# Kernel optimization log

Hardware: AMD Instinct MI355X
Metric: run time of the kernel (lower is better)

Reference implementation:

```python
import jax, jax.numpy as jnp
import numpy as np

SR = 44100
B, T = 4, SR * 3          # batch, samples (duration_secs=3)
NWT, L = 64, 512          # n_wavetables, wavetable_len


def setup_inputs() -> dict:
    key = jax.random.key(0)
    k1, k2, k3, k4, k5 = jax.random.split(key, 5)
    pitch = jax.random.uniform(k1, (B, T, 1), dtype=jnp.float32, minval=50.0, maxval=500.0)
    amplitude = jax.random.uniform(k2, (B, T, 1), dtype=jnp.float32)
    y = jax.random.normal(k3, (B, T), dtype=jnp.float32)
    wavetables = jax.random.normal(k4, (NWT, L), dtype=jnp.float32) * 0.01
    # replicate init: last sample equals first sample of each table
    wavetables = wavetables.at[:, -1].set(wavetables[:, 0])
    conv_w = jax.random.normal(k5, (1, 1, 5), dtype=jnp.float32) * 0.3  # Conv1d(1,1,5)
    conv_b = jnp.zeros((1,), dtype=jnp.float32)
    return {"pitch": pitch, "amplitude": amplitude, "y": y,
            "wavetables": wavetables, "conv_w": conv_w, "conv_b": conv_b,
            "duration_secs": 3}


def reference(pitch, amplitude, y, wavetables, conv_w, conv_b, duration_secs):
    Lwt = wavetables.shape[1]
    freq = pitch.squeeze(-1)                                   # (B, T)
    increment = freq / SR * Lwt                                # (B, T)
    # NOTE: faithful to source: subtract batch-row 0 from every row
    index = jnp.cumsum(increment, axis=1) - increment[0]
    index = index % Lwt
    idx_low = jnp.floor(index)
    idx_high = jnp.ceil(index)
    alpha = index - idx_low                                    # (B, T)
    il = idx_low.astype(jnp.int32)
    ih = idx_high.astype(jnp.int32) % Lwt
    # vectorized over all 64 wavetables at once (source loops in Python)
    low = jnp.take(wavetables, il, axis=1)                     # (N, B, T)
    high = jnp.take(wavetables, ih, axis=1)                    # (N, B, T)
    waveforms = low + alpha * (high - low)                     # (N, B, T)
    # attention: mean over batch of waveform * y
    att = jnp.mean(waveforms * y, axis=1)                      # (N, T)
    att = jax.lax.conv_general_dilated(
        att[:, None, :], conv_w, window_strides=(1,), padding=[(2, 2)],
        dimension_numbers=("NCH", "OIH", "NCH"))[:, 0, :] + conv_b[0]
    att = jax.nn.softmax(att, axis=0)                          # softmax over wavetables
    out = jnp.einsum("nbt,nt->bt", waveforms, att)             # (B, T)
    out = out[..., None] * amplitude                           # (B, T, 1)
    return out
```

## Files before the change

kernel.cpp:

```cpp
#include <hip/hip_runtime.h>
#include <math.h>

#define LWT 512
#define NWT 64
#define BB 4
#define SBASE 16
#define BLK 128
#define HALO 132


#define INC_C ((float)(512.0 / 44100.0))

__device__ __forceinline__ float inc_mul(float p) {
  float v = p * INC_C;
  asm volatile("" : "+v"(v));
  return v;
}
__device__ __forceinline__ float inc_of(const float* p, int t) { return inc_mul(p[t]); }

__global__ void __launch_bounds__(256) scan_level0(const float* __restrict__ pitch,
                                                   float* __restrict__ sarr,
                                                   float* __restrict__ s1g,
                                                   const float* __restrict__ wt,
                                                   float* __restrict__ wtT,
                                                   int T, int NB1) {
  if (blockIdx.y == BB) {
    int i = blockIdx.x * blockDim.x + threadIdx.x;
    if (i < NWT * LWT) {
      int n = i >> 9, c = i & 511;
      wtT[c * NWT + n] = wt[i];
    }
    return;
  }
  int k = blockIdx.x * blockDim.x + threadIdx.x;
  int b = blockIdx.y;
  if (k >= NB1) return;
  const float* prow = pitch + (size_t)b * T;
  float* srow = sarr + (size_t)b * T;
  int t0 = k * SBASE;
  float run = 0.0f;
  if (t0 + SBASE <= T) {
    const float4* p4 = reinterpret_cast<const float4*>(prow + t0);
    float4* s4o = reinterpret_cast<float4*>(srow + t0);
#pragma unroll
    for (int i = 0; i < 4; ++i) {
      float4 v = p4[i];
      float4 o;
      run += inc_mul(v.x); o.x = run;
      run += inc_mul(v.y); o.y = run;
      run += inc_mul(v.z); o.z = run;
      run += inc_mul(v.w); o.w = run;
      s4o[i] = o;
    }
  } else {
    for (int t = t0; t < T; ++t) { run += inc_of(prow, t); srow[t] = run; }
  }
  s1g[(size_t)b * NB1 + k] = run;
}

__global__ void __launch_bounds__(1024) scan_upper(float* __restrict__ s1g, int NB1) {
  int b = blockIdx.x;
  int tid = threadIdx.x;
  float* s1r = s1g + (size_t)b * NB1;
  __shared__ float s1[8320];
  __shared__ float s2[544];
  __shared__ float s3[48];
  __shared__ float s4[16];
  const int NB2 = (NB1 + SBASE - 1) / SBASE;
  const int NB3 = (NB2 + SBASE - 1) / SBASE;
  const int NB4 = (NB3 + SBASE - 1) / SBASE;

  for (int a = tid; a < NB1; a += 1024) s1[a] = s1r[a];
  __syncthreads();
  for (int k = tid; k < NB2; k += 1024) {
    int a0 = k * SBASE, a1 = a0 + SBASE < NB1 ? a0 + SBASE : NB1;
    float run = 0.0f;
    for (int a = a0; a < a1; ++a) { run += s1[a]; s1[a] = run; }
    s2[k] = run;
  }
  __syncthreads();
  for (int k = tid; k < NB3; k += 1024) {
    int a0 = k * SBASE, a1 = a0 + SBASE < NB2 ? a0 + SBASE : NB2;
    float run = 0.0f;
    for (int a = a0; a < a1; ++a) { run += s2[a]; s2[a] = run; }
    s3[k] = run;
  }
  __syncthreads();
  for (int k = tid; k < NB4; k += 1024) {
    int a0 = k * SBASE, a1 = a0 + SBASE < NB3 ? a0 + SBASE : NB3;
    float run = 0.0f;
    for (int a = a0; a < a1; ++a) { run += s3[a]; s3[a] = run; }
    s4[k] = run;
  }
  __syncthreads();
  if (tid == 0) { float r = 0.0f; for (int a = 0; a < NB4; ++a) { r += s4[a]; s4[a] = r; } }
  __syncthreads();
  for (int a = tid; a < NB3; a += 1024)
    if (a >= SBASE) s3[a] = s3[a] + s4[a / SBASE - 1];
  __syncthreads();
  for (int a = tid; a < NB2; a += 1024)
    if (a >= SBASE) s2[a] = s2[a] + s3[a / SBASE - 1];
  __syncthreads();
  for (int a = tid; a < NB1; a += 1024) {
    float v = s1[a];
    if (a >= SBASE) v = v + s2[a / SBASE - 1];
    s1r[a] = v;
  }
}

__device__ __forceinline__ float dpp_reduce_add(float x) {
  x += __int_as_float(__builtin_amdgcn_update_dpp(0, __float_as_int(x), 0xB1, 0xf, 0xf, true));
  x += __int_as_float(__builtin_amdgcn_update_dpp(0, __float_as_int(x), 0x4E, 0xf, 0xf, true));
  x += __int_as_float(__builtin_amdgcn_update_dpp(0, __float_as_int(x), 0x141, 0xf, 0xf, true));
  x += __int_as_float(__builtin_amdgcn_update_dpp(0, __float_as_int(x), 0x140, 0xf, 0xf, true));
  x += __int_as_float(__builtin_amdgcn_update_dpp(0, __float_as_int(x), 0x142, 0xa, 0xf, true));
  x += __int_as_float(__builtin_amdgcn_update_dpp(0, __float_as_int(x), 0x143, 0xc, 0xf, true));
  return __int_as_float(__builtin_amdgcn_readlane(__float_as_int(x), 63));
}

__global__ void __launch_bounds__(512) fused_out(
    const float* __restrict__ pitch, const float* __restrict__ sarr,
    const float* __restrict__ s1g, const float* __restrict__ y,
    const float* __restrict__ amp, const float* __restrict__ wtT,
    const float* __restrict__ cw, const float* __restrict__ cb,
    float* __restrict__ out, int T, int NB1) {
  __shared__ float lds_att[HALO][64];
  __shared__ unsigned ilh_l[BB][HALO];
  __shared__ float alf_l[BB][HALO];
  __shared__ float y_l[BB][HALO];
  __shared__ float amp_l[BB][HALO];
  __shared__ float out_l[BB][BLK];
  int t0 = blockIdx.x * BLK;
  int wid = threadIdx.x >> 6, lane = threadIdx.x & 63;

  {
    int b = wid & 3;
    for (int i = (wid >> 2) * 64 + lane; i < HALO; i += 128) {
      int t = t0 - 2 + i;
      if (t >= 0 && t < T) {
        float S = sarr[(size_t)b * T + t];
        if (t >= SBASE) S = S + s1g[b * NB1 + (t >> 4) - 1];
        float iv = S - inc_of(pitch, t);
        float q = iv * (1.0f / 512.0f);
        float k = floorf(q);
        iv = fmaf(-k, 512.0f, iv);
        float fl = floorf(iv);
        float alpha = iv - fl;
        int ili = (int)fl; if (ili > 511) ili = 511;
        int ihi = ((int)ceilf(iv)) & 511;
        ilh_l[b][i] = (unsigned)ili | ((unsigned)ihi << 16);
        alf_l[b][i] = alpha;
        y_l[b][i] = y[(size_t)b * T + t];
        amp_l[b][i] = amp[(size_t)b * T + t];
      }
    }
  }
  __syncthreads();

  for (int i = wid; i < HALO; i += 8) {
    int t = t0 - 2 + i;
    float acc = 0.0f;
    if (t >= 0 && t < T) {
#pragma unroll
      for (int b = 0; b < BB; ++b) {
        unsigned st = ilh_l[b][i];
        int ili = st & 0xffff, ihi = st >> 16;
        float alpha = alf_l[b][i];
        float lo = wtT[ili * NWT + lane];
        float hi = wtT[ihi * NWT + lane];
        acc += (lo + alpha * (hi - lo)) * y_l[b][i];
      }
      acc *= 0.25f;
    }
    lds_att[i][lane] = acc;
  }
  __syncthreads();

  float w0 = cw[0], w1 = cw[1], w2 = cw[2], w3 = cw[3], w4 = cw[4];
  float bias = cb[0];
#pragma unroll 4
  for (int i = wid; i < BLK; i += 8) {
    int t = t0 + i;
    if (t >= T) continue;
    float c = bias + lds_att[i][lane] * w0 + lds_att[i + 1][lane] * w1 +
              lds_att[i + 2][lane] * w2 + lds_att[i + 3][lane] * w3 +
              lds_att[i + 4][lane] * w4;
    float e = __expf(c);
    float r0, r1, r2, r3;
    {
      unsigned st = ilh_l[0][i + 2];
      float alpha = alf_l[0][i + 2];
      float lo = wtT[(st & 0xffff) * NWT + lane], hi = wtT[(st >> 16) * NWT + lane];
      r0 = e * (lo + alpha * (hi - lo));
    }
    {
      unsigned st = ilh_l[1][i + 2];
      float alpha = alf_l[1][i + 2];
      float lo = wtT[(st & 0xffff) * NWT + lane], hi = wtT[(st >> 16) * NWT + lane];
      r1 = e * (lo + alpha * (hi - lo));
    }
    {
      unsigned st = ilh_l[2][i + 2];
      float alpha = alf_l[2][i + 2];
      float lo = wtT[(st & 0xffff) * NWT + lane], hi = wtT[(st >> 16) * NWT + lane];
      r2 = e * (lo + alpha * (hi - lo));
    }
    {
      unsigned st = ilh_l[3][i + 2];
      float alpha = alf_l[3][i + 2];
      float lo = wtT[(st & 0xffff) * NWT + lane], hi = wtT[(st >> 16) * NWT + lane];
      r3 = e * (lo + alpha * (hi - lo));
    }
    float s0 = dpp_reduce_add(r0);
    float s1_ = dpp_reduce_add(r1);
    float s2_ = dpp_reduce_add(r2);
    float s3_ = dpp_reduce_add(r3);
    float ssum = dpp_reduce_add(e);
#if __has_builtin(__builtin_amdgcn_rcpf)
    float rc = __builtin_amdgcn_rcpf(ssum);
#else
    float rc = 1.0f / ssum;
#endif
    if (lane < BB) {
      float pv = lane == 0 ? s0 : lane == 1 ? s1_ : lane == 2 ? s2_ : s3_;
      out_l[lane][i] = pv * rc * amp_l[lane][i + 2];
    }
  }
  __syncthreads();

  {
    int b = threadIdx.x >> 7, toff = threadIdx.x & 127;
    int t = t0 + toff;
    if (t < T) out[(size_t)b * T + t] = out_l[b][toff];
  }
}

extern "C" void kernel_launch(void* const* d_in, const int* in_sizes, int n_in,
                              void* d_out, int out_size, void* d_ws, size_t ws_size,
                              hipStream_t stream) {
  const float* pitch = (const float*)d_in[0];
  const float* amp   = (const float*)d_in[1];
  const float* y     = (const float*)d_in[2];
  const float* wt    = (const float*)d_in[3];
  const float* cw    = (const float*)d_in[4];
  const float* cb    = (const float*)d_in[5];
  float* out = (float*)d_out;

  int BT = in_sizes[2];
  int T = BT / BB;
  int NB1 = (T + SBASE - 1) / SBASE;

  float* ws   = (float*)d_ws;
  float* sarr = ws;
  float* wtT  = ws + (size_t)BT;
  float* s1g  = ws + (size_t)BT + NWT * LWT;

  hipLaunchKernelGGL(scan_level0, dim3(128, BB + 1), dim3(256), 0, stream,
                     pitch, sarr, s1g, wt, wtT, T, NB1);
  hipLaunchKernelGGL(scan_upper, dim3(BB), dim3(1024), 0, stream, s1g, NB1);
  hipLaunchKernelGGL(fused_out, dim3((T + BLK - 1) / BLK), dim3(512), 0, stream,
                     pitch, sarr, s1g, y, amp, wtT, cw, cb, out, T, NB1);
}
```

Baseline: 64.37 us.

## Split upper scan into parallel level-1 kernel and shrink fused_out block tile

The scan's level-1 pass now runs as its own grid-wide kernel instead of inside a single 4-block scan_upper. scan_upper shrinks to one 256-thread block that handles levels 2-4 for all batches, and fused_out adds the level-2 prefix when it rebuilds each index. fused_out also moves to 64-sample tiles with 256 threads, giving twice as many blocks for better CU coverage. In exchange there is one more kernel launch, and the 4-sample conv halo is recomputed more often relative to each tile.

```diff
diff --git a/kernel.cpp b/kernel.cpp
--- a/kernel.cpp
+++ b/kernel.cpp
@@ -5,8 +5,8 @@
 #define NWT 64
 #define BB 4
 #define SBASE 16
-#define BLK 128
-#define HALO 132
+#define BLK 64
+#define HALO 68
 
 
 #define INC_C ((float)(512.0 / 44100.0))
@@ -58,54 +58,62 @@
   s1g[(size_t)b * NB1 + k] = run;
 }
 
-__global__ void __launch_bounds__(1024) scan_upper(float* __restrict__ s1g, int NB1) {
-  int b = blockIdx.x;
+__global__ void __launch_bounds__(256) scan_level1(float* __restrict__ s1g,
+                                                   float* __restrict__ s2g,
+                                                   int NB1, int NB2) {
+  int k = blockIdx.x * blockDim.x + threadIdx.x;
+  int b = blockIdx.y;
+  if (k >= NB2) return;
+  float* s1r = s1g + (size_t)b * NB1;
+  int a0 = k * SBASE, a1 = a0 + SBASE < NB1 ? a0 + SBASE : NB1;
+  float run = 0.0f;
+  for (int a = a0; a < a1; ++a) { run += s1r[a]; s1r[a] = run; }
+  s2g[(size_t)b * NB2 + k] = run;
+}
+
+__global__ void __launch_bounds__(256) scan_upper(float* __restrict__ s2g, int NB2) {
+  __shared__ float s2[BB][544];
+  __shared__ float s3[BB][48];
+  __shared__ float s4[BB][16];
   int tid = threadIdx.x;
-  float* s1r = s1g + (size_t)b * NB1;
-  __shared__ float s1[8320];
-  __shared__ float s2[544];
-  __shared__ float s3[48];
-  __shared__ float s4[16];
-  const int NB2 = (NB1 + SBASE - 1) / SBASE;
   const int NB3 = (NB2 + SBASE - 1) / SBASE;
   const int NB4 = (NB3 + SBASE - 1) / SBASE;
-
-  for (int a = tid; a < NB1; a += 1024) s1[a] = s1r[a];
-  __syncthreads();
-  for (int k = tid; k < NB2; k += 1024) {
-    int a0 = k * SBASE, a1 = a0 + SBASE < NB1 ? a0 + SBASE : NB1;
-    float run = 0.0f;
-    for (int a = a0; a < a1; ++a) { run += s1[a]; s1[a] = run; }
-    s2[k] = run;
-  }
-  __syncthreads();
-  for (int k = tid; k < NB3; k += 1024) {
+  for (int b = 0; b < BB; ++b)
+    for (int a = tid; a < NB2; a += 256) s2[b][a] = s2g[(size_t)b * NB2 + a];
+  __syncthreads();
+  if (tid < BB * NB3) {
+    int b = tid / NB3, k = tid % NB3;
     int a0 = k * SBASE, a1 = a0 + SBASE < NB2 ? a0 + SBASE : NB2;
     float run = 0.0f;
-    for (int a = a0; a < a1; ++a) { run += s2[a]; s2[a] = run; }
-    s3[k] = run;
-  }
-  __syncthreads();
-  for (int k = tid; k < NB4; k += 1024) {
+    for (int a = a0; a < a1; ++a) { run += s2[b][a]; s2[b][a] = run; }
+    s3[b][k] = run;
+  }
+  __syncthreads();
+  if (tid < BB * NB4) {
+    int b = tid / NB4, k = tid % NB4;
     int a0 = k * SBASE, a1 = a0 + SBASE < NB3 ? a0 + SBASE : NB3;
     float run = 0.0f;
-    for (int a = a0; a < a1; ++a) { run += s3[a]; s3[a] = run; }
-    s4[k] = run;
-  }
-  __syncthreads();
-  if (tid == 0) { float r = 0.0f; for (int a = 0; a < NB4; ++a) { r += s4[a]; s4[a] = r; } }
-  __syncthreads();
-  for (int a = tid; a < NB3; a += 1024)
-    if (a >= SBASE) s3[a] = s3[a] + s4[a / SBASE - 1];
-  __syncthreads();
-  for (int a = tid; a < NB2; a += 1024)
-    if (a >= SBASE) s2[a] = s2[a] + s3[a / SBASE - 1];
-  __syncthreads();
-  for (int a = tid; a < NB1; a += 1024) {
-    float v = s1[a];
-    if (a >= SBASE) v = v + s2[a / SBASE - 1];
-    s1r[a] = v;
-  }
+    for (int a = a0; a < a1; ++a) { run += s3[b][a]; s3[b][a] = run; }
+    s4[b][k] = run;
+  }
+  __syncthreads();
+  if (tid < BB) {
+    int b = tid;
+    float r = 0.0f;
+    for (int a = 0; a < NB4; ++a) { r += s4[b][a]; s4[b][a] = r; }
+  }
+  __syncthreads();
+  if (tid < BB * NB3) {
+    int b = tid / NB3, a = tid % NB3;
+    if (a >= SBASE) s3[b][a] = s3[b][a] + s4[b][a / SBASE - 1];
+  }
+  __syncthreads();
+  for (int b = 0; b < BB; ++b)
+    for (int a = tid; a < NB2; a += 256) {
+      float v = s2[b][a];
+      if (a >= SBASE) v = v + s3[b][a / SBASE - 1];
+      s2g[(size_t)b * NB2 + a] = v;
+    }
 }
 
 __device__ __forceinline__ float dpp_reduce_add(float x) {
@@ -118,28 +126,34 @@
   return __int_as_float(__builtin_amdgcn_readlane(__float_as_int(x), 63));
 }
 
-__global__ void __launch_bounds__(512) fused_out(
+__global__ void __launch_bounds__(256) fused_out(
     const float* __restrict__ pitch, const float* __restrict__ sarr,
-    const float* __restrict__ s1g, const float* __restrict__ y,
-    const float* __restrict__ amp, const float* __restrict__ wtT,
-    const float* __restrict__ cw, const float* __restrict__ cb,
-    float* __restrict__ out, int T, int NB1) {
+    const float* __restrict__ s1g, const float* __restrict__ s2g,
+    const float* __restrict__ y, const float* __restrict__ amp,
+    const float* __restrict__ wtT, const float* __restrict__ cw,
+    const float* __restrict__ cb, float* __restrict__ out,
+    int T, int NB1, int NB2) {
   __shared__ float lds_att[HALO][64];
   __shared__ unsigned ilh_l[BB][HALO];
   __shared__ float alf_l[BB][HALO];
   __shared__ float y_l[BB][HALO];
   __shared__ float amp_l[BB][HALO];
-  __shared__ float out_l[BB][BLK];
+  __shared__ float out_l[BB][BLK + 1];
   int t0 = blockIdx.x * BLK;
   int wid = threadIdx.x >> 6, lane = threadIdx.x & 63;
 
   {
-    int b = wid & 3;
-    for (int i = (wid >> 2) * 64 + lane; i < HALO; i += 128) {
+    int b = wid;
+    for (int i = lane; i < HALO; i += 64) {
       int t = t0 - 2 + i;
       if (t >= 0 && t < T) {
         float S = sarr[(size_t)b * T + t];
-        if (t >= SBASE) S = S + s1g[b * NB1 + (t >> 4) - 1];
+        if (t >= SBASE) {
+          int k1 = (t >> 4) - 1;
+          float s1v = s1g[b * NB1 + k1];
+          if (k1 >= SBASE) s1v = s1v + s2g[b * NB2 + (k1 >> 4) - 1];
+          S = S + s1v;
+        }
         float iv = S - inc_of(pitch, t);
         float q = iv * (1.0f / 512.0f);
         float k = floorf(q);
@@ -157,7 +171,7 @@
   }
   __syncthreads();
 
-  for (int i = wid; i < HALO; i += 8) {
+  for (int i = wid; i < HALO; i += 4) {
     int t = t0 - 2 + i;
     float acc = 0.0f;
     if (t >= 0 && t < T) {
@@ -179,7 +193,7 @@
   float w0 = cw[0], w1 = cw[1], w2 = cw[2], w3 = cw[3], w4 = cw[4];
   float bias = cb[0];
 #pragma unroll 4
-  for (int i = wid; i < BLK; i += 8) {
+  for (int i = wid; i < BLK; i += 4) {
     int t = t0 + i;
     if (t >= T) continue;
     float c = bias + lds_att[i][lane] * w0 + lds_att[i + 1][lane] * w1 +
@@ -229,9 +243,9 @@
   __syncthreads();
 
   {
-    int b = threadIdx.x >> 7, toff = threadIdx.x & 127;
-    int t = t0 + toff;
-    if (t < T) out[(size_t)b * T + t] = out_l[b][toff];
+    int b = wid;
+    int t = t0 + lane;
+    if (t < T) out[(size_t)b * T + t] = out_l[b][lane];
   }
 }
 
@@ -249,15 +263,19 @@
   int BT = in_sizes[2];
   int T = BT / BB;
   int NB1 = (T + SBASE - 1) / SBASE;
+  int NB2 = (NB1 + SBASE - 1) / SBASE;
 
   float* ws   = (float*)d_ws;
   float* sarr = ws;
   float* wtT  = ws + (size_t)BT;
   float* s1g  = ws + (size_t)BT + NWT * LWT;
+  float* s2g  = s1g + (size_t)BB * NB1;
 
   hipLaunchKernelGGL(scan_level0, dim3(128, BB + 1), dim3(256), 0, stream,
                      pitch, sarr, s1g, wt, wtT, T, NB1);
-  hipLaunchKernelGGL(scan_upper, dim3(BB), dim3(1024), 0, stream, s1g, NB1);
-  hipLaunchKernelGGL(fused_out, dim3((T + BLK - 1) / BLK), dim3(512), 0, stream,
-                     pitch, sarr, s1g, y, amp, wtT, cw, cb, out, T, NB1);
-}
+  hipLaunchKernelGGL(scan_level1, dim3((NB2 + 255) / 256, BB), dim3(256), 0, stream,
+                     s1g, s2g, NB1, NB2);
+  hipLaunchKernelGGL(scan_upper, dim3(1), dim3(256), 0, stream, s2g, NB2);
+  hipLaunchKernelGGL(fused_out, dim3((T + BLK - 1) / BLK), dim3(256), 0, stream,
+                     pitch, sarr, s1g, s2g, y, amp, wtT, cw, cb, out, T, NB1, NB2);
+}
```

Measured after the change: 62.75 us. -2.5%, faster.
